# Performance work log

Hardware: AMD Instinct MI355X
Metric: run time of the kernel (lower is better)

## Reference

```python
import jax, jax.numpy as jnp
import numpy as np

# Quantization constants from the original module
X_SCALE, X_ZP = 0.0215, -25
Y_SCALE, Y_ZP = 0.0176, 18


def setup_inputs() -> dict:
    key = jax.random.key(0)
    kx, ky = jax.random.split(key)
    K, N = 8192, 16384
    # int8 stand-ins (enum lacks int8); values fit int8 range
    x = jax.random.randint(kx, (K,), 0, 127, dtype=jnp.int32)
    y = jax.random.randint(ky, (K, N), 0, 127, dtype=jnp.int32)
    return {"x": x, "y": y}


def reference(x, y):
    # dequantize_per_tensor: (q - zero_point) * scale, in fp32
    xf = (x.astype(jnp.float32) - X_ZP) * X_SCALE   # [K]
    yf = (y.astype(jnp.float32) - Y_ZP) * Y_SCALE   # [K, N]
    # vector-matrix matmul -> [N]
    return xf @ yf
```

## Files before the change

kernel.cpp:

```cpp
#include <hip/hip_runtime.h>


constexpr int K = 8192;
constexpr int N = 16384;
constexpr float X_SCALE = 0.0215f;
constexpr int   X_ZP    = -25;
constexpr float Y_SCALE = 0.0176f;
constexpr int   Y_ZP    = 18;

constexpr int BLOCK = 256;
constexpr int VEC   = 4;
constexpr int COLS_PER_BLOCK = BLOCK * VEC;
constexpr int NBLK_N = N / COLS_PER_BLOCK;
constexpr int SPLIT_K = 64;
constexpr int KCHUNK = K / SPLIT_K;

__global__ void zero_out_kernel(float* __restrict__ out) {
    int i = blockIdx.x * blockDim.x + threadIdx.x;
    if (i < N) out[i] = 0.0f;
}

__global__ __launch_bounds__(BLOCK) void qgemv_kernel(const int* __restrict__ x,
                                                      const int* __restrict__ y,
                                                      float* __restrict__ out) {
    __shared__ int xs[KCHUNK];

    const int nb = blockIdx.x % NBLK_N;
    const int kc = blockIdx.x / NBLK_N;
    const int k0 = kc * KCHUNK;

    for (int i = threadIdx.x; i < KCHUNK; i += BLOCK)
        xs[i] = x[k0 + i] - X_ZP;
    __syncthreads();

    const int col = nb * COLS_PER_BLOCK + threadIdx.x * VEC;
    const int4* yv = (const int4*)(y + (size_t)k0 * N + col);
    const size_t stride4 = N / VEC;

    int acc0 = 0, acc1 = 0, acc2 = 0, acc3 = 0;
    int sx = 0;

#pragma unroll 8
    for (int k = 0; k < KCHUNK; ++k) {
        int4 v = yv[(size_t)k * stride4];
        int a = xs[k];
        sx   += a;
        acc0 += a * v.x;
        acc1 += a * v.y;
        acc2 += a * v.z;
        acc3 += a * v.w;
    }

    const float sxy = X_SCALE * Y_SCALE;
    const int corr = Y_ZP * sx;
    atomicAdd(&out[col + 0], sxy * (float)(acc0 - corr));
    atomicAdd(&out[col + 1], sxy * (float)(acc1 - corr));
    atomicAdd(&out[col + 2], sxy * (float)(acc2 - corr));
    atomicAdd(&out[col + 3], sxy * (float)(acc3 - corr));
}

extern "C" void kernel_launch(void* const* d_in, const int* in_sizes, int n_in,
                              void* d_out, int out_size, void* d_ws, size_t ws_size,
                              hipStream_t stream) {
    const int* x = (const int*)d_in[0];
    const int* y = (const int*)d_in[1];
    float* out = (float*)d_out;

    zero_out_kernel<<<(N + 255) / 256, 256, 0, stream>>>(out);
    qgemv_kernel<<<NBLK_N * SPLIT_K, BLOCK, 0, stream>>>(x, y, out);
}
```

Before: 679.4 us.

## Replace atomic split-K reduction with workspace partials and deterministic reduce kernel

Partial kernel writes exact int32 partial sums per K-chunk to a workspace instead of float atomics into the output, and a second kernel reduces the 64 partials and scales. This removes the zeroing kernel and atomic contention. The partial kernel also uses nontemporal loads for the streamed matrix, unroll 16, and a launch bound hint of 4 blocks. It adds a 4 MB workspace round trip and requires d_ws to be large enough.

```diff
diff --git a/kernel.cpp b/kernel.cpp
--- a/kernel.cpp
+++ b/kernel.cpp
@@ -14,15 +14,13 @@
 constexpr int NBLK_N = N / COLS_PER_BLOCK;
 constexpr int SPLIT_K = 64;
 constexpr int KCHUNK = K / SPLIT_K;
+constexpr int N4 = N / 4;
 
-__global__ void zero_out_kernel(float* __restrict__ out) {
-    int i = blockIdx.x * blockDim.x + threadIdx.x;
-    if (i < N) out[i] = 0.0f;
-}
+typedef int ivec4 __attribute__((ext_vector_type(4)));
 
-__global__ __launch_bounds__(BLOCK) void qgemv_kernel(const int* __restrict__ x,
-                                                      const int* __restrict__ y,
-                                                      float* __restrict__ out) {
+__global__ __launch_bounds__(BLOCK, 4) void qgemv_partial(const int* __restrict__ x,
+                                                          const ivec4* __restrict__ y,
+                                                          ivec4* __restrict__ ws) {
     __shared__ int xs[KCHUNK];
 
     const int nb = blockIdx.x % NBLK_N;
@@ -33,16 +31,15 @@
         xs[i] = x[k0 + i] - X_ZP;
     __syncthreads();
 
-    const int col = nb * COLS_PER_BLOCK + threadIdx.x * VEC;
-    const int4* yv = (const int4*)(y + (size_t)k0 * N + col);
-    const size_t stride4 = N / VEC;
+    const int col4 = nb * (COLS_PER_BLOCK / 4) + threadIdx.x;
+    const ivec4* yv = y + (size_t)k0 * N4 + col4;
 
     int acc0 = 0, acc1 = 0, acc2 = 0, acc3 = 0;
     int sx = 0;
 
-#pragma unroll 8
+#pragma unroll 16
     for (int k = 0; k < KCHUNK; ++k) {
-        int4 v = yv[(size_t)k * stride4];
+        ivec4 v = __builtin_nontemporal_load(&yv[(size_t)k * N4]);
         int a = xs[k];
         sx   += a;
         acc0 += a * v.x;
@@ -51,21 +48,41 @@
         acc3 += a * v.w;
     }
 
-    const float sxy = X_SCALE * Y_SCALE;
     const int corr = Y_ZP * sx;
-    atomicAdd(&out[col + 0], sxy * (float)(acc0 - corr));
-    atomicAdd(&out[col + 1], sxy * (float)(acc1 - corr));
-    atomicAdd(&out[col + 2], sxy * (float)(acc2 - corr));
-    atomicAdd(&out[col + 3], sxy * (float)(acc3 - corr));
+    ivec4 p;
+    p.x = acc0 - corr;
+    p.y = acc1 - corr;
+    p.z = acc2 - corr;
+    p.w = acc3 - corr;
+    ws[(size_t)kc * N4 + col4] = p;
+}
+
+__global__ __launch_bounds__(BLOCK) void qgemv_reduce(const ivec4* __restrict__ ws,
+                                                      float* __restrict__ out) {
+    const int t = blockIdx.x * BLOCK + threadIdx.x;
+    int sx = 0, sy = 0, sz = 0, sw = 0;
+#pragma unroll 8
+    for (int kc = 0; kc < SPLIT_K; ++kc) {
+        ivec4 v = ws[(size_t)kc * N4 + t];
+        sx += v.x; sy += v.y; sz += v.z; sw += v.w;
+    }
+    const float s = X_SCALE * Y_SCALE;
+    float4 o;
+    o.x = s * (float)sx;
+    o.y = s * (float)sy;
+    o.z = s * (float)sz;
+    o.w = s * (float)sw;
+    ((float4*)out)[t] = o;
 }
 
 extern "C" void kernel_launch(void* const* d_in, const int* in_sizes, int n_in,
                               void* d_out, int out_size, void* d_ws, size_t ws_size,
                               hipStream_t stream) {
     const int* x = (const int*)d_in[0];
-    const int* y = (const int*)d_in[1];
+    const ivec4* y = (const ivec4*)d_in[1];
     float* out = (float*)d_out;
+    ivec4* ws = (ivec4*)d_ws;
 
-    zero_out_kernel<<<(N + 255) / 256, 256, 0, stream>>>(out);
-    qgemv_kernel<<<NBLK_N * SPLIT_K, BLOCK, 0, stream>>>(x, y, out);
+    qgemv_partial<<<NBLK_N * SPLIT_K, BLOCK, 0, stream>>>(x, y, ws);
+    qgemv_reduce<<<N4 / BLOCK, BLOCK, 0, stream>>>(ws, out);
 }
```

Measured after the change: 673.9 us. About the same (-0.8%).
